# Optimization experiments

Measured on AMD Instinct MI355X. Metric: run time of the kernel, lower is better.

Reference implementation:

```python
import jax, jax.numpy as jnp
import numpy as np

B, S, E, H = 4, 2048, 1024, 16
D = E // H  # head dim = 64


def setup_inputs() -> dict:
    key = jax.random.key(0)
    ks = jax.random.split(key, 5)
    s = 0.02
    return {
        "x": jax.random.normal(ks[0], (B, S, E), dtype=jnp.float32),
        "Wq": jax.random.normal(ks[1], (E, E), dtype=jnp.float32) * s,
        "Wk": jax.random.normal(ks[2], (E, E), dtype=jnp.float32) * s,
        "Wv": jax.random.normal(ks[3], (E, E), dtype=jnp.float32) * s,
        "Wo": jax.random.normal(ks[4], (E, E), dtype=jnp.float32) * s,
        "bo": jnp.zeros((E,), dtype=jnp.float32),
    }


def reference(x, Wq, Wk, Wv, Wo, bo):
    b, s, e = x.shape
    h, d = H, e // H
    # QKV projections -> [b, h, s, d]
    q = (x @ Wq).reshape(b, s, h, d).transpose(0, 2, 1, 3)
    k = (x @ Wk).reshape(b, s, h, d).transpose(0, 2, 1, 3)
    v = (x @ Wv).reshape(b, s, h, d).transpose(0, 2, 1, 3)
    # scores [b, h, s, s], causal mask with -inf, scaled softmax
    a = jnp.einsum('bhqd,bhkd->bhqk', q, k)
    causal = jnp.tril(jnp.ones((s, s), dtype=bool))  # True where allowed
    a = jnp.where(causal, a, -jnp.inf) / jnp.sqrt(jnp.asarray(d, x.dtype))
    a = jax.nn.softmax(a, axis=-1)
    # dropout p=0.0 (identity in eval)
    y = jnp.einsum('bhqk,bhkd->bhqd', a, v)
    y = y.transpose(0, 2, 1, 3).reshape(b, s, e)
    return y @ Wo + bo
```

## Files before the change

kernel.cpp:

```cpp
#include <hip/hip_runtime.h>

typedef __bf16 bf16x8 __attribute__((ext_vector_type(8)));
typedef float f32x4 __attribute__((ext_vector_type(4)));

#define S_LEN 2048
#define NHEAD 16
#define HDIM  64
#define EMB   1024

__device__ __forceinline__ ushort f2b(float v) {
  union { float f; unsigned u; } x; x.f = v;
  unsigned r = (x.u + 0x7fffu + ((x.u >> 16) & 1u)) >> 16;
  return (ushort)r;
}

__device__ __forceinline__ ushort f2b_trunc(float v) {
  union { float f; unsigned u; } x; x.f = v;
  return (ushort)(x.u >> 16);
}

typedef const __attribute__((address_space(1))) unsigned int* gp1_t;
typedef __attribute__((address_space(3))) unsigned int* lp3_t;
__device__ __forceinline__ void gld16(const ushort* g, const ushort* l) {
  __builtin_amdgcn_global_load_lds((gp1_t)(unsigned long long)(uintptr_t)g,
                                   (lp3_t)(unsigned int)(uintptr_t)l, 16, 0, 0);
}

__global__ __launch_bounds__(256) void cast_x_kernel(const float* __restrict__ x,
                                                     ushort* __restrict__ xb) {
  size_t i = ((size_t)blockIdx.x * 256 + threadIdx.x) * 4;
  float4 v = *(const float4*)(x + i);
  ushort4 o;
  o.x = f2b(v.x); o.y = f2b(v.y); o.z = f2b(v.z); o.w = f2b(v.w);
  *(ushort4*)(xb + i) = o;
}

__global__ __launch_bounds__(256) void tcast_w_kernel(const float* __restrict__ W0,
                                                      const float* __restrict__ W1,
                                                      const float* __restrict__ W2,
                                                      const float* __restrict__ W3,
                                                      ushort* __restrict__ Wt0,
                                                      ushort* __restrict__ Wt1,
                                                      ushort* __restrict__ Wt2,
                                                      ushort* __restrict__ Wt3,
                                                      float scale0) {
  __shared__ float t[32][33];
  const int z = blockIdx.z;
  const float* W = z == 0 ? W0 : (z == 1 ? W1 : (z == 2 ? W2 : W3));
  ushort* Wt = z == 0 ? Wt0 : (z == 1 ? Wt1 : (z == 2 ? Wt2 : Wt3));
  const float scale = z == 0 ? scale0 : 1.0f;
  int k0 = blockIdx.x * 32, n0 = blockIdx.y * 32;
  int c = threadIdx.x & 31, r0 = threadIdx.x >> 5;
#pragma unroll
  for (int i = 0; i < 4; ++i) {
    int r = r0 + i * 8;
    t[r][c] = W[(size_t)(k0 + r) * EMB + n0 + c];
  }
  __syncthreads();
#pragma unroll
  for (int i = 0; i < 4; ++i) {
    int r = r0 + i * 8;
    Wt[(size_t)(n0 + r) * EMB + k0 + c] = f2b(t[c][r] * scale);
  }
}

__global__ __launch_bounds__(256) void transpose_v_kernel(const ushort* __restrict__ V,
                                                          ushort* __restrict__ Vt) {
  __shared__ ushort t[32][33];
  int s0 = blockIdx.x * 32, d0 = blockIdx.y * 32;
  size_t base = (size_t)blockIdx.z * S_LEN * HDIM;
  int c = threadIdx.x & 31, r0 = threadIdx.x >> 5;
#pragma unroll
  for (int i = 0; i < 4; ++i) {
    int r = r0 + i * 8;
    t[r][c] = V[base + (size_t)(s0 + r) * HDIM + d0 + c];
  }
  __syncthreads();
#pragma unroll
  for (int i = 0; i < 4; ++i) {
    int r = r0 + i * 8;
    Vt[base + (size_t)(d0 + r) * S_LEN + s0 + c] = t[c][r];
  }
}

template <int EPI>
__global__ __launch_bounds__(256) void gemm_kernel(
    const ushort* __restrict__ A, const ushort* __restrict__ Bt, int K, int N,
    ushort* __restrict__ outQ, ushort* __restrict__ outK, ushort* __restrict__ outV,
    float* __restrict__ outF, const float* __restrict__ bias) {
  __shared__ ushort As[2][128 * 32];
  __shared__ ushort Bs[2][128 * 32];
  const int tid = threadIdx.x;
  const int lane = tid & 63, ln = lane & 15, quad = lane >> 4;
  const int wave = tid >> 6, wm = wave >> 1, wn = wave & 1;
  const long m0 = (long)blockIdx.x * 128, n0 = (long)blockIdx.y * 128;

  const int sr = lane >> 2, sc = (lane & 3) * 8;
  const ushort* AgL = A + (m0 + 32 * wave + sr) * (long)K + sc;
  const ushort* BgL = Bt + (n0 + 32 * wave + sr) * (long)K + sc;

  f32x4 acc[4][4] = {};
  const int KT = K >> 5;

  {
    ushort* as = &As[0][32 * wave * 32];
    ushort* bs = &Bs[0][32 * wave * 32];
    gld16(AgL, as);
    gld16(AgL + 16 * (long)K, as + 16 * 32);
    gld16(BgL, bs);
    gld16(BgL + 16 * (long)K, bs + 16 * 32);
  }
  __syncthreads();

  for (int kt = 0; kt < KT; ++kt) {
    if (kt + 1 < KT) {
      const int nb = (kt + 1) & 1;
      const ushort* a = AgL + (kt + 1) * 32;
      const ushort* b = BgL + (kt + 1) * 32;
      ushort* as = &As[nb][32 * wave * 32];
      ushort* bs = &Bs[nb][32 * wave * 32];
      gld16(a, as);
      gld16(a + 16 * (long)K, as + 16 * 32);
      gld16(b, bs);
      gld16(b + 16 * (long)K, bs + 16 * 32);
    }
    const ushort* Ac = &As[kt & 1][0];
    const ushort* Bc = &Bs[kt & 1][0];
    bf16x8 af[4], bf[4];
#pragma unroll
    for (int mt = 0; mt < 4; ++mt)
      af[mt] = *(const bf16x8*)(Ac + (wm * 64 + mt * 16 + ln) * 32 + quad * 8);
#pragma unroll
    for (int nt = 0; nt < 4; ++nt)
      bf[nt] = *(const bf16x8*)(Bc + (wn * 64 + nt * 16 + ln) * 32 + quad * 8);
#pragma unroll
    for (int mt = 0; mt < 4; ++mt)
#pragma unroll
      for (int nt = 0; nt < 4; ++nt)
        acc[mt][nt] = __builtin_amdgcn_mfma_f32_16x16x32_bf16(af[mt], bf[nt], acc[mt][nt], 0, 0, 0);
    __syncthreads();
  }

#pragma unroll
  for (int mt = 0; mt < 4; ++mt) {
#pragma unroll
    for (int nt = 0; nt < 4; ++nt) {
#pragma unroll
      for (int r = 0; r < 4; ++r) {
        long m = m0 + wm * 64 + mt * 16 + quad * 4 + r;
        long n = n0 + wn * 64 + nt * 16 + ln;
        float v = acc[mt][nt][r];
        if (EPI == 0) {
          int sel = (int)(n >> 10);
          int nn = (int)(n & 1023);
          int h = nn >> 6, d = nn & 63;
          long b = m >> 11, s = m & 2047;
          ushort* dst = sel == 0 ? outQ : (sel == 1 ? outK : outV);
          dst[(((b * NHEAD + h) * S_LEN) + s) * HDIM + d] = f2b(v);
        } else {
          outF[m * (long)N + n] = v + bias[n];
        }
      }
    }
  }
}

__global__ __launch_bounds__(256) void attn_kernel(const ushort* __restrict__ Q,
                                                   const ushort* __restrict__ Kg,
                                                   const ushort* __restrict__ Vt,
                                                   ushort* __restrict__ Y) {
  __shared__ ushort Ks[2][2 * 64 * 32];
  __shared__ ushort Vs[2][2 * 64 * 32];
  __shared__ ushort Ps[4 * 2 * 16 * 72];
  const int tid = threadIdx.x;
  const int wave = tid >> 6, lane = tid & 63, ln = lane & 15, quad = lane >> 4;
  const int bh = blockIdx.x;
  const int qb = 15 - (int)blockIdx.y;
  const int q0 = qb * 128;
  const size_t base = (size_t)bh * S_LEN * HDIM;
  const int ntiles = 2 * qb + 2;

  bf16x8 qf[2][2];
#pragma unroll
  for (int mt = 0; mt < 2; ++mt)
#pragma unroll
    for (int ks2 = 0; ks2 < 2; ++ks2)
      qf[mt][ks2] = *(const bf16x8*)(Q + base + (size_t)(q0 + wave * 32 + mt * 16 + ln) * HDIM +
                                     ks2 * 32 + quad * 8);

  f32x4 acc[2][4] = {};
  float l_part[2][4] = {};

  const int sr = lane >> 2, sc = (lane & 3) * 8;
  const ushort* KgL = Kg + base + (size_t)(16 * wave + sr) * HDIM + sc;
  const ushort* VgL = Vt + base + (size_t)(16 * wave + sr) * S_LEN + sc;

  {
    ushort* kb = &Ks[0][16 * wave * 32];
    ushort* vb = &Vs[0][16 * wave * 32];
    gld16(KgL, kb);
    gld16(KgL + 32, kb + 2048);
    gld16(VgL, vb);
    gld16(VgL + 32, vb + 2048);
  }
  __syncthreads();

  ushort* Pw0 = Ps + wave * 2304;
  ushort* Pw1 = Pw0 + 1152;

  for (int kt = 0; kt < ntiles; ++kt) {
    const int cur = kt & 1;
    const int k0 = kt * 64;
    if (kt + 1 < ntiles) {
      const int nb = cur ^ 1;
      const size_t k1 = (size_t)(k0 + 64);
      ushort* kb = &Ks[nb][16 * wave * 32];
      ushort* vb = &Vs[nb][16 * wave * 32];
      gld16(KgL + k1 * HDIM, kb);
      gld16(KgL + k1 * HDIM + 32, kb + 2048);
      gld16(VgL + k1, vb);
      gld16(VgL + k1 + 32, vb + 2048);
    }
    const ushort* Kc = &Ks[cur][0];
    const ushort* Vc = &Vs[cur][0];
    const int qbase = q0 + wave * 32;

    if (k0 < qbase + 32) {
      f32x4 s0[4] = {}, s1[4] = {};
#pragma unroll
      for (int ks2 = 0; ks2 < 2; ++ks2) {
#pragma unroll
        for (int nt = 0; nt < 4; ++nt) {
          bf16x8 bk = *(const bf16x8*)(Kc + ks2 * 2048 + (nt * 16 + ln) * 32 + quad * 8);
          s0[nt] = __builtin_amdgcn_mfma_f32_16x16x32_bf16(qf[0][ks2], bk, s0[nt], 0, 0, 0);
          s1[nt] = __builtin_amdgcn_mfma_f32_16x16x32_bf16(qf[1][ks2], bk, s1[nt], 0, 0, 0);
        }
      }

      if (k0 + 63 > qbase) {
        const int rowq = qbase + quad * 4;
#pragma unroll
        for (int nt = 0; nt < 4; ++nt)
#pragma unroll
          for (int r = 0; r < 4; ++r) {
            const int key = k0 + nt * 16 + ln;
            if (key > rowq + r) s0[nt][r] = -3.0e38f;
            if (key > rowq + 16 + r) s1[nt][r] = -3.0e38f;
          }
      }

      asm volatile("" ::: "memory");
#pragma unroll
      for (int nt = 0; nt < 4; ++nt) {
#pragma unroll
        for (int r = 0; r < 4; ++r) {
          float p0 = __builtin_amdgcn_exp2f(s0[nt][r]);
          float p1 = __builtin_amdgcn_exp2f(s1[nt][r]);
          l_part[0][r] += p0;
          l_part[1][r] += p1;
          Pw0[(quad * 4 + r) * 72 + nt * 16 + ln] = f2b_trunc(p0);
          Pw1[(quad * 4 + r) * 72 + nt * 16 + ln] = f2b_trunc(p1);
        }
      }
      asm volatile("" ::: "memory");

#pragma unroll
      for (int ks2 = 0; ks2 < 2; ++ks2) {
        bf16x8 ap0 = *(const bf16x8*)(Pw0 + ln * 72 + ks2 * 32 + quad * 8);
        bf16x8 ap1 = *(const bf16x8*)(Pw1 + ln * 72 + ks2 * 32 + quad * 8);
#pragma unroll
        for (int t2 = 0; t2 < 4; ++t2) {
          bf16x8 bv = *(const bf16x8*)(Vc + ks2 * 2048 + (t2 * 16 + ln) * 32 + quad * 8);
          acc[0][t2] = __builtin_amdgcn_mfma_f32_16x16x32_bf16(ap0, bv, acc[0][t2], 0, 0, 0);
          acc[1][t2] = __builtin_amdgcn_mfma_f32_16x16x32_bf16(ap1, bv, acc[1][t2], 0, 0, 0);
        }
      }
    }
    __syncthreads();
  }

  const long b = bh >> 4;
  const int h = bh & 15;
#pragma unroll
  for (int mt = 0; mt < 2; ++mt) {
#pragma unroll
    for (int r = 0; r < 4; ++r) {
      float t = l_part[mt][r];
      t += __shfl_xor(t, 1);
      t += __shfl_xor(t, 2);
      t += __shfl_xor(t, 4);
      t += __shfl_xor(t, 8);
      float inv = 1.0f / t;
      const int qq = q0 + wave * 32 + mt * 16 + quad * 4 + r;
#pragma unroll
      for (int t2 = 0; t2 < 4; ++t2)
        Y[(((b * S_LEN + qq) * NHEAD) + h) * HDIM + t2 * 16 + ln] = f2b(acc[mt][t2][r] * inv);
    }
  }
}

extern "C" void kernel_launch(void* const* d_in, const int* in_sizes, int n_in,
                              void* d_out, int out_size, void* d_ws, size_t ws_size,
                              hipStream_t stream) {
  const float* x  = (const float*)d_in[0];
  const float* Wq = (const float*)d_in[1];
  const float* Wk = (const float*)d_in[2];
  const float* Wv = (const float*)d_in[3];
  const float* Wo = (const float*)d_in[4];
  const float* bo = (const float*)d_in[5];
  float* out = (float*)d_out;

  const size_t NTOK = (size_t)4 * S_LEN;
  const size_t XE = NTOK * EMB;
  ushort* ws    = (ushort*)d_ws;
  ushort* xb    = ws;
  ushort* Wtqkv = xb + XE;
  ushort* Wto   = Wtqkv + 3 * 1048576;
  ushort* Qb    = Wto + 1048576;
  ushort* Kb    = Qb + XE;
  ushort* Vb    = Kb + XE;
  ushort* Vtb   = Vb + XE;
  ushort* Yb    = xb;

  const float SCALE_Q = 1.4426950408889634f / 8.0f;

  cast_x_kernel<<<8192, 256, 0, stream>>>(x, xb);
  tcast_w_kernel<<<dim3(32, 32, 4), 256, 0, stream>>>(
      Wq, Wk, Wv, Wo, Wtqkv, Wtqkv + 1048576, Wtqkv + 2097152, Wto, SCALE_Q);

  gemm_kernel<0><<<dim3(64, 24), 256, 0, stream>>>(xb, Wtqkv, EMB, 3072,
                                                   Qb, Kb, Vb, nullptr, nullptr);
  transpose_v_kernel<<<dim3(64, 2, 64), 256, 0, stream>>>(Vb, Vtb);
  attn_kernel<<<dim3(64, 16), 256, 0, stream>>>(Qb, Kb, Vtb, Yb);
  gemm_kernel<1><<<dim3(64, 8), 256, 0, stream>>>(Yb, Wto, EMB, EMB,
                                                  nullptr, nullptr, nullptr, out, bo);
}
```

Baseline: 249.9 us.

## Fuse prep casts, write V transposed from GEMM, MFMA row sums, swizzle P

Merges the x cast and the weight transpose-casts into a single prep kernel. The QKV GEMM epilogue now writes V directly in transposed layout with packed 8-byte stores, so the separate transpose kernel and its extra V buffer are removed. In attention, the softmax denominators are computed by an MFMA against a ones vector instead of scalar adds and cross-lane shuffles, and the P scratch tile uses an XOR swizzle to cut LDS bank conflicts. This saves two launches and a full V round trip through memory, at the cost of two extra MFMAs per step and denominators that are summed from bf16-rounded probabilities.

```diff
diff --git a/kernel.cpp b/kernel.cpp
--- a/kernel.cpp
+++ b/kernel.cpp
@@ -2,6 +2,7 @@
 
 typedef __bf16 bf16x8 __attribute__((ext_vector_type(8)));
 typedef float f32x4 __attribute__((ext_vector_type(4)));
+typedef unsigned short u16x8 __attribute__((ext_vector_type(8)));
 
 #define S_LEN 2048
 #define NHEAD 16
@@ -26,26 +27,25 @@
                                    (lp3_t)(unsigned int)(uintptr_t)l, 16, 0, 0);
 }
 
-__global__ __launch_bounds__(256) void cast_x_kernel(const float* __restrict__ x,
-                                                     ushort* __restrict__ xb) {
-  size_t i = ((size_t)blockIdx.x * 256 + threadIdx.x) * 4;
-  float4 v = *(const float4*)(x + i);
-  ushort4 o;
-  o.x = f2b(v.x); o.y = f2b(v.y); o.z = f2b(v.z); o.w = f2b(v.w);
-  *(ushort4*)(xb + i) = o;
-}
-
-__global__ __launch_bounds__(256) void tcast_w_kernel(const float* __restrict__ W0,
-                                                      const float* __restrict__ W1,
-                                                      const float* __restrict__ W2,
-                                                      const float* __restrict__ W3,
-                                                      ushort* __restrict__ Wt0,
-                                                      ushort* __restrict__ Wt1,
-                                                      ushort* __restrict__ Wt2,
-                                                      ushort* __restrict__ Wt3,
-                                                      float scale0) {
+__global__ __launch_bounds__(256) void prep_kernel(
+    const float* __restrict__ x, const float* __restrict__ W0,
+    const float* __restrict__ W1, const float* __restrict__ W2,
+    const float* __restrict__ W3, ushort* __restrict__ xb,
+    ushort* __restrict__ Wt0, ushort* __restrict__ Wt1,
+    ushort* __restrict__ Wt2, ushort* __restrict__ Wt3, float scale0) {
+  const int z = blockIdx.z;
+  if (z == 4) {
+    size_t base = ((size_t)(blockIdx.y * 32 + blockIdx.x)) * 8192 + threadIdx.x * 4;
+#pragma unroll
+    for (int i = 0; i < 8; ++i) {
+      float4 v = *(const float4*)(x + base + i * 1024);
+      ushort4 o;
+      o.x = f2b(v.x); o.y = f2b(v.y); o.z = f2b(v.z); o.w = f2b(v.w);
+      *(ushort4*)(xb + base + i * 1024) = o;
+    }
+    return;
+  }
   __shared__ float t[32][33];
-  const int z = blockIdx.z;
   const float* W = z == 0 ? W0 : (z == 1 ? W1 : (z == 2 ? W2 : W3));
   ushort* Wt = z == 0 ? Wt0 : (z == 1 ? Wt1 : (z == 2 ? Wt2 : Wt3));
   const float scale = z == 0 ? scale0 : 1.0f;
@@ -64,29 +64,10 @@
   }
 }
 
-__global__ __launch_bounds__(256) void transpose_v_kernel(const ushort* __restrict__ V,
-                                                          ushort* __restrict__ Vt) {
-  __shared__ ushort t[32][33];
-  int s0 = blockIdx.x * 32, d0 = blockIdx.y * 32;
-  size_t base = (size_t)blockIdx.z * S_LEN * HDIM;
-  int c = threadIdx.x & 31, r0 = threadIdx.x >> 5;
-#pragma unroll
-  for (int i = 0; i < 4; ++i) {
-    int r = r0 + i * 8;
-    t[r][c] = V[base + (size_t)(s0 + r) * HDIM + d0 + c];
-  }
-  __syncthreads();
-#pragma unroll
-  for (int i = 0; i < 4; ++i) {
-    int r = r0 + i * 8;
-    Vt[base + (size_t)(d0 + r) * S_LEN + s0 + c] = t[c][r];
-  }
-}
-
 template <int EPI>
 __global__ __launch_bounds__(256) void gemm_kernel(
     const ushort* __restrict__ A, const ushort* __restrict__ Bt, int K, int N,
-    ushort* __restrict__ outQ, ushort* __restrict__ outK, ushort* __restrict__ outV,
+    ushort* __restrict__ outQ, ushort* __restrict__ outK, ushort* __restrict__ outVt,
     float* __restrict__ outF, const float* __restrict__ bias) {
   __shared__ ushort As[2][128 * 32];
   __shared__ ushort Bs[2][128 * 32];
@@ -141,24 +122,50 @@
     __syncthreads();
   }
 
-#pragma unroll
-  for (int mt = 0; mt < 4; ++mt) {
-#pragma unroll
-    for (int nt = 0; nt < 4; ++nt) {
-#pragma unroll
-      for (int r = 0; r < 4; ++r) {
-        long m = m0 + wm * 64 + mt * 16 + quad * 4 + r;
-        long n = n0 + wn * 64 + nt * 16 + ln;
-        float v = acc[mt][nt][r];
-        if (EPI == 0) {
-          int sel = (int)(n >> 10);
-          int nn = (int)(n & 1023);
-          int h = nn >> 6, d = nn & 63;
-          long b = m >> 11, s = m & 2047;
-          ushort* dst = sel == 0 ? outQ : (sel == 1 ? outK : outV);
-          dst[(((b * NHEAD + h) * S_LEN) + s) * HDIM + d] = f2b(v);
-        } else {
-          outF[m * (long)N + n] = v + bias[n];
+  if (EPI == 0) {
+    const int sel = (int)(n0 >> 10);
+    if (sel == 2) {
+#pragma unroll
+      for (int mt = 0; mt < 4; ++mt) {
+        const long mbase = m0 + wm * 64 + mt * 16 + quad * 4;
+        const long bb = mbase >> 11, s = mbase & 2047;
+#pragma unroll
+        for (int nt = 0; nt < 4; ++nt) {
+          const int nn = (int)((n0 & 1023) + wn * 64 + nt * 16 + ln);
+          const int h = nn >> 6, d = nn & 63;
+          uint2 val;
+          val.x = (unsigned)f2b(acc[mt][nt][0]) | ((unsigned)f2b(acc[mt][nt][1]) << 16);
+          val.y = (unsigned)f2b(acc[mt][nt][2]) | ((unsigned)f2b(acc[mt][nt][3]) << 16);
+          *(uint2*)(outVt + (((bb * NHEAD + h) * (long)HDIM + d) * S_LEN) + s) = val;
+        }
+      }
+    } else {
+      ushort* dst = sel == 0 ? outQ : outK;
+#pragma unroll
+      for (int mt = 0; mt < 4; ++mt) {
+#pragma unroll
+        for (int nt = 0; nt < 4; ++nt) {
+          const int nn = (int)((n0 & 1023) + wn * 64 + nt * 16 + ln);
+          const int h = nn >> 6, d = nn & 63;
+#pragma unroll
+          for (int r = 0; r < 4; ++r) {
+            const long m = m0 + wm * 64 + mt * 16 + quad * 4 + r;
+            const long bb = m >> 11, s = m & 2047;
+            dst[(((bb * NHEAD + h) * S_LEN) + s) * HDIM + d] = f2b(acc[mt][nt][r]);
+          }
+        }
+      }
+    }
+  } else {
+#pragma unroll
+    for (int mt = 0; mt < 4; ++mt) {
+#pragma unroll
+      for (int nt = 0; nt < 4; ++nt) {
+#pragma unroll
+        for (int r = 0; r < 4; ++r) {
+          const long m = m0 + wm * 64 + mt * 16 + quad * 4 + r;
+          const long n = n0 + wn * 64 + nt * 16 + ln;
+          outF[m * (long)N + n] = acc[mt][nt][r] + bias[n];
         }
       }
     }
@@ -169,9 +176,9 @@
                                                    const ushort* __restrict__ Kg,
                                                    const ushort* __restrict__ Vt,
                                                    ushort* __restrict__ Y) {
-  __shared__ ushort Ks[2][2 * 64 * 32];
-  __shared__ ushort Vs[2][2 * 64 * 32];
-  __shared__ ushort Ps[4 * 2 * 16 * 72];
+  __shared__ alignas(16) ushort Ks[2][2 * 64 * 32];
+  __shared__ alignas(16) ushort Vs[2][2 * 64 * 32];
+  __shared__ alignas(16) ushort Ps[4 * 2 * 16 * 72];
   const int tid = threadIdx.x;
   const int wave = tid >> 6, lane = tid & 63, ln = lane & 15, quad = lane >> 4;
   const int bh = blockIdx.x;
@@ -180,6 +187,9 @@
   const size_t base = (size_t)bh * S_LEN * HDIM;
   const int ntiles = 2 * qb + 2;
 
+  const u16x8 ob = {0x3F80, 0x3F80, 0x3F80, 0x3F80, 0x3F80, 0x3F80, 0x3F80, 0x3F80};
+  const bf16x8 ones = __builtin_bit_cast(bf16x8, ob);
+
   bf16x8 qf[2][2];
 #pragma unroll
   for (int mt = 0; mt < 2; ++mt)
@@ -189,7 +199,7 @@
                                      ks2 * 32 + quad * 8);
 
   f32x4 acc[2][4] = {};
-  float l_part[2][4] = {};
+  f32x4 accl[2] = {};
 
   const int sr = lane >> 2, sc = (lane & 3) * 8;
   const ushort* KgL = Kg + base + (size_t)(16 * wave + sr) * HDIM + sc;
@@ -207,6 +217,8 @@
 
   ushort* Pw0 = Ps + wave * 2304;
   ushort* Pw1 = Pw0 + 1152;
+  const int swW = (quad >> 1) << 4;
+  const int swR = (ln >> 3) << 4;
 
   for (int kt = 0; kt < ntiles; ++kt) {
     const int cur = kt & 1;
@@ -256,18 +268,21 @@
         for (int r = 0; r < 4; ++r) {
           float p0 = __builtin_amdgcn_exp2f(s0[nt][r]);
           float p1 = __builtin_amdgcn_exp2f(s1[nt][r]);
-          l_part[0][r] += p0;
-          l_part[1][r] += p1;
-          Pw0[(quad * 4 + r) * 72 + nt * 16 + ln] = f2b_trunc(p0);
-          Pw1[(quad * 4 + r) * 72 + nt * 16 + ln] = f2b_trunc(p1);
+          const int row = (quad * 4 + r) * 72;
+          const int col = (nt * 16 + ln) ^ swW;
+          Pw0[row + col] = f2b_trunc(p0);
+          Pw1[row + col] = f2b_trunc(p1);
         }
       }
       asm volatile("" ::: "memory");
 
 #pragma unroll
       for (int ks2 = 0; ks2 < 2; ++ks2) {
-        bf16x8 ap0 = *(const bf16x8*)(Pw0 + ln * 72 + ks2 * 32 + quad * 8);
-        bf16x8 ap1 = *(const bf16x8*)(Pw1 + ln * 72 + ks2 * 32 + quad * 8);
+        const int rcol = (ks2 * 32 + quad * 8) ^ swR;
+        bf16x8 ap0 = *(const bf16x8*)(Pw0 + ln * 72 + rcol);
+        bf16x8 ap1 = *(const bf16x8*)(Pw1 + ln * 72 + rcol);
+        accl[0] = __builtin_amdgcn_mfma_f32_16x16x32_bf16(ap0, ones, accl[0], 0, 0, 0);
+        accl[1] = __builtin_amdgcn_mfma_f32_16x16x32_bf16(ap1, ones, accl[1], 0, 0, 0);
 #pragma unroll
         for (int t2 = 0; t2 < 4; ++t2) {
           bf16x8 bv = *(const bf16x8*)(Vc + ks2 * 2048 + (t2 * 16 + ln) * 32 + quad * 8);
@@ -285,12 +300,7 @@
   for (int mt = 0; mt < 2; ++mt) {
 #pragma unroll
     for (int r = 0; r < 4; ++r) {
-      float t = l_part[mt][r];
-      t += __shfl_xor(t, 1);
-      t += __shfl_xor(t, 2);
-      t += __shfl_xor(t, 4);
-      t += __shfl_xor(t, 8);
-      float inv = 1.0f / t;
+      float inv = 1.0f / accl[mt][r];
       const int qq = q0 + wave * 32 + mt * 16 + quad * 4 + r;
 #pragma unroll
       for (int t2 = 0; t2 < 4; ++t2)
@@ -310,27 +320,23 @@
   const float* bo = (const float*)d_in[5];
   float* out = (float*)d_out;
 
-  const size_t NTOK = (size_t)4 * S_LEN;
-  const size_t XE = NTOK * EMB;
+  const size_t XE = (size_t)8192 * EMB;
   ushort* ws    = (ushort*)d_ws;
   ushort* xb    = ws;
   ushort* Wtqkv = xb + XE;
   ushort* Wto   = Wtqkv + 3 * 1048576;
   ushort* Qb    = Wto + 1048576;
   ushort* Kb    = Qb + XE;
-  ushort* Vb    = Kb + XE;
-  ushort* Vtb   = Vb + XE;
+  ushort* Vtb   = Kb + XE;
   ushort* Yb    = xb;
 
   const float SCALE_Q = 1.4426950408889634f / 8.0f;
 
-  cast_x_kernel<<<8192, 256, 0, stream>>>(x, xb);
-  tcast_w_kernel<<<dim3(32, 32, 4), 256, 0, stream>>>(
-      Wq, Wk, Wv, Wo, Wtqkv, Wtqkv + 1048576, Wtqkv + 2097152, Wto, SCALE_Q);
+  prep_kernel<<<dim3(32, 32, 5), 256, 0, stream>>>(
+      x, Wq, Wk, Wv, Wo, xb, Wtqkv, Wtqkv + 1048576, Wtqkv + 2097152, Wto, SCALE_Q);
 
   gemm_kernel<0><<<dim3(64, 24), 256, 0, stream>>>(xb, Wtqkv, EMB, 3072,
-                                                   Qb, Kb, Vb, nullptr, nullptr);
-  transpose_v_kernel<<<dim3(64, 2, 64), 256, 0, stream>>>(Vb, Vtb);
+                                                   Qb, Kb, Vtb, nullptr, nullptr);
   attn_kernel<<<dim3(64, 16), 256, 0, stream>>>(Qb, Kb, Vtb, Yb);
   gemm_kernel<1><<<dim3(64, 8), 256, 0, stream>>>(Yb, Wto, EMB, EMB,
                                                   nullptr, nullptr, nullptr, out, bo);
```

Measured after the change: 238.1 us. -4.7%, faster.
